# Kernel optimization log

Hardware: AMD Instinct MI355X
Metric: run time of the kernel (lower is better)

The kernel has to match this reference:

```python
import jax, jax.numpy as jnp
import numpy as np

B, H, L, D = 2, 16, 2048, 64

def setup_inputs() -> dict:
    key = jax.random.key(0)
    kq, kk, kv, km = jax.random.split(key, 4)
    q = jax.random.normal(kq, (B, H, L, D), dtype=jnp.float32)
    k = jax.random.normal(kk, (B, H, L, D), dtype=jnp.float32)
    v = jax.random.normal(kv, (B, H, L, D), dtype=jnp.float32)
    mask = jax.random.randint(km, (B, 1, L, L), 0, 2, dtype=jnp.int32)
    return {"q": q, "k": k, "v": v, "mask": mask}

def reference(q, k, v, mask):
    d_tensor = q.shape[-1]
    # score: [B,H,L,L] = q @ k^T / sqrt(d)
    score = jnp.einsum("bhqd,bhkd->bhqk", q, k) / jnp.sqrt(jnp.float32(d_tensor))
    score = jnp.where(mask == 0, jnp.float32(-jnp.inf), score)
    score = jax.nn.softmax(score, axis=-1)
    # torch.nan_to_num(nan=0.0): rows fully masked produce NaN -> 0
    score = jnp.where(jnp.isnan(score), jnp.float32(0.0), score)
    # dropout=0.0 (eval / p=0) -> identity
    out = jnp.einsum("bhqk,bhkd->bhqd", score, v)
    return (out, score)
```

## Files before the change

### kernel.cpp

```cpp
#include <hip/hip_runtime.h>
#include <math.h>

#define B_ 2
#define H_ 16
#define L_ 2048
#define D_ 64
#define OUT_ELEMS ((size_t)B_ * H_ * L_ * D_)
#define WPR (L_ / 16)
#define C1 0.180336880f

typedef _Float16 half8 __attribute__((ext_vector_type(8)));
typedef _Float16 half4_t __attribute__((ext_vector_type(4)));
typedef float f32x4 __attribute__((ext_vector_type(4)));
typedef int i32x4 __attribute__((ext_vector_type(4)));
typedef unsigned int u32;
typedef unsigned short u16;
typedef u16 u16x4 __attribute__((ext_vector_type(4)));
typedef u32 u32x4 __attribute__((ext_vector_type(4)));
typedef u32 u32x2 __attribute__((ext_vector_type(2)));

#define SWZ(row, colh) ((colh) ^ (((row) & 7) << 3))

__global__ __launch_bounds__(256) void pack_kernel(
    const int* __restrict__ M, u16* __restrict__ pmask)
{
  const int idx = blockIdx.x * 256 + threadIdx.x;
  const int* src = M + (size_t)idx * 16;
  u32 w = 0;
#pragma unroll
  for (int j = 0; j < 4; ++j) {
    i32x4 m = ((const i32x4*)src)[j];
#pragma unroll
    for (int r = 0; r < 4; ++r)
      w |= (m[r] != 0 ? 1u : 0u) << (j * 4 + r);
  }
  pmask[idx] = (u16)w;
}

__global__ __launch_bounds__(256, 4) void lsum_kernel(
    const float* __restrict__ Q, const float* __restrict__ K,
    const u16* __restrict__ pmask, float* __restrict__ lpart)
{
  const int qt = blockIdx.x, h = blockIdx.y;
  const int b = blockIdx.z >> 2, kq = blockIdx.z & 3;
  const int bh = b * H_ + h;
  const int q0 = qt * 64, k0 = kq * 512;
  const int tid = threadIdx.x;
  const int wv = tid >> 6, lane = tid & 63;
  const int lr = lane & 15, lg = lane >> 4;
  const int qrow = q0 + wv * 16 + lr;

  __shared__ _Float16 Kbuf[2][64 * 64];

  const float* kbase = K + ((size_t)bh * L_ + k0) * D_;
  const u16* pmrow = pmask + (size_t)(b * L_ + qrow) * WPR + (k0 >> 4);

  half8 qf[2];
  {
    const float* qr = Q + (size_t)(bh * L_ + qrow) * D_;
#pragma unroll
    for (int f = 0; f < 2; ++f) {
      f32x4 x = *(const f32x4*)(qr + f * 32 + lg * 8);
      f32x4 y = *(const f32x4*)(qr + f * 32 + lg * 8 + 4);
      qf[f] = half8{(_Float16)(x[0]*C1), (_Float16)(x[1]*C1), (_Float16)(x[2]*C1), (_Float16)(x[3]*C1),
                    (_Float16)(y[0]*C1), (_Float16)(y[1]*C1), (_Float16)(y[2]*C1), (_Float16)(y[3]*C1)};
    }
  }

  const int ksr = tid >> 2, ksd = (tid & 3) * 16;
  auto loadK4 = [&](int kc, f32x4* r) {
    const float* s = kbase + (size_t)(kc + ksr) * D_ + ksd;
    r[0] = ((const f32x4*)s)[0]; r[1] = ((const f32x4*)s)[1];
    r[2] = ((const f32x4*)s)[2]; r[3] = ((const f32x4*)s)[3];
  };
  auto writeK = [&](int buf, const f32x4* r) {
    half8 lo = half8{(_Float16)r[0][0], (_Float16)r[0][1], (_Float16)r[0][2], (_Float16)r[0][3],
                     (_Float16)r[1][0], (_Float16)r[1][1], (_Float16)r[1][2], (_Float16)r[1][3]};
    half8 hi = half8{(_Float16)r[2][0], (_Float16)r[2][1], (_Float16)r[2][2], (_Float16)r[2][3],
                     (_Float16)r[3][0], (_Float16)r[3][1], (_Float16)r[3][2], (_Float16)r[3][3]};
    *(half8*)&Kbuf[buf][(ksr << 6) + SWZ(ksr, ksd)] = lo;
    *(half8*)&Kbuf[buf][(ksr << 6) + SWZ(ksr, ksd + 8)] = hi;
  };

  float l_l = 0.f;
  {
    f32x4 kr[4];
    loadK4(0, kr);
    writeK(0, kr);
  }
  __syncthreads();

  for (int c = 0; c < 8; ++c) {
    const int kc = c * 64, cur = c & 1;
    f32x4 kr[4];
    if (c < 7) loadK4(kc + 64, kr);
    u16x4 pm = *(const u16x4*)(pmrow + c * 4);

    f32x4 acc[4] = {f32x4{0,0,0,0}, f32x4{0,0,0,0}, f32x4{0,0,0,0}, f32x4{0,0,0,0}};
    __builtin_amdgcn_s_setprio(1);
#pragma unroll
    for (int kb = 0; kb < 4; ++kb) {
      int row = kb * 16 + lr;
      half8 a0 = *(const half8*)&Kbuf[cur][(row << 6) + SWZ(row, lg * 8)];
      half8 a1 = *(const half8*)&Kbuf[cur][(row << 6) + SWZ(row, 32 + lg * 8)];
      acc[kb] = __builtin_amdgcn_mfma_f32_16x16x32_f16(a0, qf[0], acc[kb], 0, 0, 0);
      acc[kb] = __builtin_amdgcn_mfma_f32_16x16x32_f16(a1, qf[1], acc[kb], 0, 0, 0);
    }
    __builtin_amdgcn_s_setprio(0);

    float cs = 0.f;
#pragma unroll
    for (int kb = 0; kb < 4; ++kb)
#pragma unroll
      for (int r = 0; r < 4; ++r)
        cs += exp2f(((pm[kb] >> (lg * 4 + r)) & 1) ? acc[kb][r] : -INFINITY);
    l_l += cs;

    if (c < 7) writeK(cur ^ 1, kr);
    __syncthreads();
  }

  l_l += __shfl_xor(l_l, 16);
  l_l += __shfl_xor(l_l, 32);
  if (lg == 0)
    lpart[((size_t)kq * 32 + bh) * L_ + qrow] = l_l;
}

template <int KCH>
__device__ __forceinline__ void attn_body(
    const float* Q, const float* K, const float* V,
    const u16* pmask, const float* lpart,
    float* obase, float* score, int b, int h, int qt, int k0)
{
  const int bh = b * H_ + h;
  const int q0 = qt * 64;
  const int tid = threadIdx.x;
  const int wv = tid >> 6, lane = tid & 63;
  const int lr = lane & 15, lg = lane >> 4;
  const int qrow = q0 + wv * 16 + lr;

  __shared__ _Float16 Klds[2][64 * 64];
  __shared__ _Float16 Vlds[2][64 * 64];

  const float* kbase = K + ((size_t)bh * L_ + k0) * D_;
  const float* vbase = V + ((size_t)bh * L_ + k0) * D_;
  const u16* pmrow = pmask + (size_t)(b * L_ + qrow) * WPR + (k0 >> 4);
  float* srow = score + ((size_t)bh * L_ + qrow) * L_ + k0;
  float* ob = obase + (size_t)(bh * L_ + q0) * D_;

  float lsum = 0.f;
#pragma unroll
  for (int kq = 0; kq < 4; ++kq)
    lsum += lpart[((size_t)kq * 32 + bh) * L_ + qrow];
  const float inv_l = (lsum > 0.f) ? 1.f / lsum : 0.f;

  half8 qf[2];
  {
    const float* qr = Q + (size_t)(bh * L_ + qrow) * D_;
#pragma unroll
    for (int f = 0; f < 2; ++f) {
      f32x4 x = *(const f32x4*)(qr + f * 32 + lg * 8);
      f32x4 y = *(const f32x4*)(qr + f * 32 + lg * 8 + 4);
      qf[f] = half8{(_Float16)(x[0]*C1), (_Float16)(x[1]*C1), (_Float16)(x[2]*C1), (_Float16)(x[3]*C1),
                    (_Float16)(y[0]*C1), (_Float16)(y[1]*C1), (_Float16)(y[2]*C1), (_Float16)(y[3]*C1)};
    }
  }

  const int ksr = tid >> 2, ksd = (tid & 3) * 16;
  const int vk0 = (tid & 15) * 4, vd0 = (tid >> 4) * 4;

  auto loadK4 = [&](int kc, f32x4* r) {
    const float* s = kbase + (size_t)(kc + ksr) * D_ + ksd;
    r[0] = ((const f32x4*)s)[0]; r[1] = ((const f32x4*)s)[1];
    r[2] = ((const f32x4*)s)[2]; r[3] = ((const f32x4*)s)[3];
  };
  auto writeK = [&](int buf, const f32x4* r) {
    half8 lo = half8{(_Float16)r[0][0], (_Float16)r[0][1], (_Float16)r[0][2], (_Float16)r[0][3],
                     (_Float16)r[1][0], (_Float16)r[1][1], (_Float16)r[1][2], (_Float16)r[1][3]};
    half8 hi = half8{(_Float16)r[2][0], (_Float16)r[2][1], (_Float16)r[2][2], (_Float16)r[2][3],
                     (_Float16)r[3][0], (_Float16)r[3][1], (_Float16)r[3][2], (_Float16)r[3][3]};
    *(half8*)&Klds[buf][(ksr << 6) + SWZ(ksr, ksd)] = lo;
    *(half8*)&Klds[buf][(ksr << 6) + SWZ(ksr, ksd + 8)] = hi;
  };
  auto loadV4 = [&](int kc, f32x4* r) {
#pragma unroll
    for (int i = 0; i < 4; ++i)
      r[i] = *(const f32x4*)(vbase + (size_t)(kc + vk0 + i) * D_ + vd0);
  };
  auto writeV = [&](int buf, const f32x4* r) {
#pragma unroll
    for (int j = 0; j < 4; ++j) {
      int row = vd0 + j;
      *(half4_t*)&Vlds[buf][(row << 6) + SWZ(row, vk0)] =
          half4_t{(_Float16)r[0][j], (_Float16)r[1][j],
                  (_Float16)r[2][j], (_Float16)r[3][j]};
    }
  };

  {
    f32x4 kr[4], vr[4];
    loadK4(0, kr); loadV4(0, vr);
    writeK(0, kr); writeV(0, vr);
  }
  __syncthreads();

  f32x4 o_acc[4] = {f32x4{0,0,0,0}, f32x4{0,0,0,0}, f32x4{0,0,0,0}, f32x4{0,0,0,0}};

  const int s0lane = lr + 32 * (lg & 1);
  const int s1lane = s0lane + 16;
  const bool hisel = (lg & 2) != 0;

  for (int c = 0; c < KCH; ++c) {
    const int kc = c * 64, cur = c & 1;
    f32x4 krP[4], vrP[4];
    if (c < KCH - 1) {
      loadK4(kc + 64, krP);
      loadV4(kc + 64, vrP);
    }
    u16x4 pm = *(const u16x4*)(pmrow + c * 4);

    f32x4 acc[4] = {f32x4{0,0,0,0}, f32x4{0,0,0,0}, f32x4{0,0,0,0}, f32x4{0,0,0,0}};
    __builtin_amdgcn_s_setprio(1);
#pragma unroll
    for (int kb = 0; kb < 4; ++kb) {
      int row = kb * 16 + lr;
      half8 a0 = *(const half8*)&Klds[cur][(row << 6) + SWZ(row, lg * 8)];
      half8 a1 = *(const half8*)&Klds[cur][(row << 6) + SWZ(row, 32 + lg * 8)];
      acc[kb] = __builtin_amdgcn_mfma_f32_16x16x32_f16(a0, qf[0], acc[kb], 0, 0, 0);
      acc[kb] = __builtin_amdgcn_mfma_f32_16x16x32_f16(a1, qf[1], acc[kb], 0, 0, 0);
    }
    __builtin_amdgcn_s_setprio(0);

    u32 phu[8];
#pragma unroll
    for (int kb = 0; kb < 4; ++kb) {
      f32x4 p4;
#pragma unroll
      for (int r = 0; r < 4; ++r)
        p4[r] = exp2f(((pm[kb] >> (lg * 4 + r)) & 1) ? acc[kb][r] : -INFINITY) * inv_l;
      __builtin_nontemporal_store(p4, (f32x4*)(srow + kc + kb * 16 + lg * 4));
      half4_t hp = half4_t{(_Float16)p4[0], (_Float16)p4[1],
                           (_Float16)p4[2], (_Float16)p4[3]};
      u32x2 uu = __builtin_bit_cast(u32x2, hp);
      phu[2 * kb] = uu[0];
      phu[2 * kb + 1] = uu[1];
    }

    __builtin_amdgcn_s_setprio(1);
#pragma unroll
    for (int ks = 0; ks < 2; ++ks) {
      int a0 = __shfl((int)phu[4 * ks + 0], s0lane);
      int a1 = __shfl((int)phu[4 * ks + 1], s0lane);
      int a2 = __shfl((int)phu[4 * ks + 2], s0lane);
      int a3 = __shfl((int)phu[4 * ks + 3], s0lane);
      int b0 = __shfl((int)phu[4 * ks + 0], s1lane);
      int b1 = __shfl((int)phu[4 * ks + 1], s1lane);
      int b2 = __shfl((int)phu[4 * ks + 2], s1lane);
      int b3 = __shfl((int)phu[4 * ks + 3], s1lane);
      u32x4 pau = u32x4{(u32)(hisel ? a2 : a0), (u32)(hisel ? a3 : a1),
                        (u32)(hisel ? b2 : b0), (u32)(hisel ? b3 : b1)};
      half8 pa = __builtin_bit_cast(half8, pau);
#pragma unroll
      for (int db = 0; db < 4; ++db) {
        int row = db * 16 + lr;
        half8 vf = *(const half8*)&Vlds[cur][(row << 6) + SWZ(row, ks * 32 + lg * 8)];
        o_acc[db] = __builtin_amdgcn_mfma_f32_16x16x32_f16(pa, vf, o_acc[db], 0, 0, 0);
      }
    }
    __builtin_amdgcn_s_setprio(0);

    if (c < KCH - 1) {
      writeK(cur ^ 1, krP);
      writeV(cur ^ 1, vrP);
    }
    __syncthreads();
  }

#pragma unroll
  for (int db = 0; db < 4; ++db)
#pragma unroll
    for (int r = 0; r < 4; ++r)
      ob[(size_t)(wv * 16 + lg * 4 + r) * D_ + db * 16 + lr] = o_acc[db][r];
}

__global__ __launch_bounds__(256, 4) void attn_split_kernel(
    const float* __restrict__ Q, const float* __restrict__ K,
    const float* __restrict__ V, const u16* __restrict__ pmask,
    const float* __restrict__ lpart,
    float* __restrict__ op0, float* __restrict__ op1, float* __restrict__ score)
{
  const int bid = blockIdx.x;
  const int lid = (bid & 7) * (2048 / 8) + (bid >> 3);
  const int qt = lid & 31, kh = (lid >> 5) & 1, h = (lid >> 6) & 15, b = lid >> 10;
  attn_body<16>(Q, K, V, pmask, lpart, kh ? op1 : op0, score,
                b, h, qt, kh * 1024);
}

__global__ __launch_bounds__(256, 4) void attn_full_kernel(
    const float* __restrict__ Q, const float* __restrict__ K,
    const float* __restrict__ V, const u16* __restrict__ pmask,
    const float* __restrict__ lpart,
    float* __restrict__ out, float* __restrict__ score)
{
  const int bid = blockIdx.x;
  const int lid = (bid & 7) * (1024 / 8) + (bid >> 3);
  const int qt = lid & 31, h = (lid >> 5) & 15, b = lid >> 9;
  attn_body<32>(Q, K, V, pmask, lpart, out, score, b, h, qt, 0);
}

__global__ __launch_bounds__(256) void combine_kernel(
    const float* __restrict__ op1, float* __restrict__ out)
{
  const int idx = blockIdx.x * 256 + threadIdx.x;
  f32x4 a = ((const f32x4*)out)[idx];
  f32x4 bq = ((const f32x4*)op1)[idx];
  a[0] += bq[0]; a[1] += bq[1]; a[2] += bq[2]; a[3] += bq[3];
  __builtin_nontemporal_store(a, (f32x4*)out + idx);
}

extern "C" void kernel_launch(void* const* d_in, const int* in_sizes, int n_in,
                              void* d_out, int out_size, void* d_ws, size_t ws_size,
                              hipStream_t stream) {
  const float* q = (const float*)d_in[0];
  const float* k = (const float*)d_in[1];
  const float* v = (const float*)d_in[2];
  const int* mask = (const int*)d_in[3];
  float* out = (float*)d_out;
  float* score = out + OUT_ELEMS;

  u16* pmask = (u16*)d_ws;
  float* lpart = (float*)((char*)d_ws + (1 << 20));
  float* op1 = (float*)((char*)d_ws + (2 << 20));
  const size_t need = (size_t)(2 << 20) + OUT_ELEMS * sizeof(float);

  pack_kernel<<<dim3(B_ * L_ * WPR / 256), 256, 0, stream>>>(mask, pmask);
  lsum_kernel<<<dim3(32, 16, 8), 256, 0, stream>>>(q, k, pmask, lpart);
  if (ws_size >= need) {
    attn_split_kernel<<<dim3(2048), 256, 0, stream>>>(q, k, v, pmask, lpart,
                                                      out, op1, score);
    combine_kernel<<<dim3(OUT_ELEMS / 4 / 256), 256, 0, stream>>>(op1, out);
  } else {
    attn_full_kernel<<<dim3(1024), 256, 0, stream>>>(q, k, v, pmask, lpart,
                                                     out, score);
  }
}
```

Before: 244.5 us.

## Single-buffer K tile in lsum kernel and raise occupancy target to 8

Replaces the register-prefetched double-buffered K tile in lsum_kernel with a single LDS buffer that is loaded, converted and stored each iteration between two barriers. Launch bounds go from 4 to 8 blocks per CU. The aim is to halve LDS use and register pressure so more waves stay resident and hide latency through occupancy instead of software pipelining. In exchange each chunk now waits on its global load before computing and pays an extra barrier.

```diff
diff --git a/kernel.cpp b/kernel.cpp
--- a/kernel.cpp
+++ b/kernel.cpp
@@ -37,7 +37,7 @@
   pmask[idx] = (u16)w;
 }
 
-__global__ __launch_bounds__(256, 4) void lsum_kernel(
+__global__ __launch_bounds__(256, 8) void lsum_kernel(
     const float* __restrict__ Q, const float* __restrict__ K,
     const u16* __restrict__ pmask, float* __restrict__ lpart)
 {
@@ -50,7 +50,7 @@
   const int lr = lane & 15, lg = lane >> 4;
   const int qrow = q0 + wv * 16 + lr;
 
-  __shared__ _Float16 Kbuf[2][64 * 64];
+  __shared__ _Float16 Kbuf[64 * 64];
 
   const float* kbase = K + ((size_t)bh * L_ + k0) * D_;
   const u16* pmrow = pmask + (size_t)(b * L_ + qrow) * WPR + (k0 >> 4);
@@ -68,41 +68,35 @@
   }
 
   const int ksr = tid >> 2, ksd = (tid & 3) * 16;
-  auto loadK4 = [&](int kc, f32x4* r) {
-    const float* s = kbase + (size_t)(kc + ksr) * D_ + ksd;
-    r[0] = ((const f32x4*)s)[0]; r[1] = ((const f32x4*)s)[1];
-    r[2] = ((const f32x4*)s)[2]; r[3] = ((const f32x4*)s)[3];
-  };
-  auto writeK = [&](int buf, const f32x4* r) {
-    half8 lo = half8{(_Float16)r[0][0], (_Float16)r[0][1], (_Float16)r[0][2], (_Float16)r[0][3],
-                     (_Float16)r[1][0], (_Float16)r[1][1], (_Float16)r[1][2], (_Float16)r[1][3]};
-    half8 hi = half8{(_Float16)r[2][0], (_Float16)r[2][1], (_Float16)r[2][2], (_Float16)r[2][3],
-                     (_Float16)r[3][0], (_Float16)r[3][1], (_Float16)r[3][2], (_Float16)r[3][3]};
-    *(half8*)&Kbuf[buf][(ksr << 6) + SWZ(ksr, ksd)] = lo;
-    *(half8*)&Kbuf[buf][(ksr << 6) + SWZ(ksr, ksd + 8)] = hi;
-  };
-
   float l_l = 0.f;
-  {
+
+  for (int c = 0; c < 8; ++c) {
+    const int kc = c * 64;
     f32x4 kr[4];
-    loadK4(0, kr);
-    writeK(0, kr);
-  }
-  __syncthreads();
-
-  for (int c = 0; c < 8; ++c) {
-    const int kc = c * 64, cur = c & 1;
-    f32x4 kr[4];
-    if (c < 7) loadK4(kc + 64, kr);
+    {
+      const float* s = kbase + (size_t)(kc + ksr) * D_ + ksd;
+      kr[0] = ((const f32x4*)s)[0]; kr[1] = ((const f32x4*)s)[1];
+      kr[2] = ((const f32x4*)s)[2]; kr[3] = ((const f32x4*)s)[3];
+    }
+    __syncthreads();
+    {
+      half8 lo = half8{(_Float16)kr[0][0], (_Float16)kr[0][1], (_Float16)kr[0][2], (_Float16)kr[0][3],
+                       (_Float16)kr[1][0], (_Float16)kr[1][1], (_Float16)kr[1][2], (_Float16)kr[1][3]};
+      half8 hi = half8{(_Float16)kr[2][0], (_Float16)kr[2][1], (_Float16)kr[2][2], (_Float16)kr[2][3],
+                       (_Float16)kr[3][0], (_Float16)kr[3][1], (_Float16)kr[3][2], (_Float16)kr[3][3]};
+      *(half8*)&Kbuf[(ksr << 6) + SWZ(ksr, ksd)] = lo;
+      *(half8*)&Kbuf[(ksr << 6) + SWZ(ksr, ksd + 8)] = hi;
+    }
+    __syncthreads();
+
     u16x4 pm = *(const u16x4*)(pmrow + c * 4);
-
     f32x4 acc[4] = {f32x4{0,0,0,0}, f32x4{0,0,0,0}, f32x4{0,0,0,0}, f32x4{0,0,0,0}};
     __builtin_amdgcn_s_setprio(1);
 #pragma unroll
     for (int kb = 0; kb < 4; ++kb) {
       int row = kb * 16 + lr;
-      half8 a0 = *(const half8*)&Kbuf[cur][(row << 6) + SWZ(row, lg * 8)];
-      half8 a1 = *(const half8*)&Kbuf[cur][(row << 6) + SWZ(row, 32 + lg * 8)];
+      half8 a0 = *(const half8*)&Kbuf[(row << 6) + SWZ(row, lg * 8)];
+      half8 a1 = *(const half8*)&Kbuf[(row << 6) + SWZ(row, 32 + lg * 8)];
       acc[kb] = __builtin_amdgcn_mfma_f32_16x16x32_f16(a0, qf[0], acc[kb], 0, 0, 0);
       acc[kb] = __builtin_amdgcn_mfma_f32_16x16x32_f16(a1, qf[1], acc[kb], 0, 0, 0);
     }
@@ -115,9 +109,6 @@
       for (int r = 0; r < 4; ++r)
         cs += exp2f(((pm[kb] >> (lg * 4 + r)) & 1) ? acc[kb][r] : -INFINITY);
     l_l += cs;
-
-    if (c < 7) writeK(cur ^ 1, kr);
-    __syncthreads();
   }
 
   l_l += __shfl_xor(l_l, 16);
```

New measurement: 242.2 us. About the same (-1.0%).
